# Kernel tuning notes

Hardware: AMD Instinct MI355X
Metric: run time of the kernel (lower is better)

The kernel has to match this reference:

```python
import jax, jax.numpy as jnp
import numpy as np

IGNORE = 255


def interp_bilinear_ac(x, H, W):
    """Bilinear interpolation with align_corners=True. x: [B,C,h,w] -> [B,C,H,W]."""
    B, C, h, w = x.shape

    def coords(n_in, n_out):
        s = jnp.linspace(0.0, n_in - 1.0, n_out)
        i0 = jnp.clip(jnp.floor(s).astype(jnp.int32), 0, n_in - 2)
        t = (s - i0).astype(x.dtype)
        return i0, t

    y0, ty = coords(h, H)
    x = x[:, :, y0, :] * (1.0 - ty)[None, None, :, None] + x[:, :, y0 + 1, :] * ty[None, None, :, None]
    x0, tx = coords(w, W)
    x = x[:, :, :, x0] * (1.0 - tx) + x[:, :, :, x0 + 1] * tx
    return x


def cross_entropy(logits, labels):
    """Mean CE over valid pixels. logits: [B,C,H,W], labels: [B,H,W] int."""
    C = logits.shape[1]
    logp = jax.nn.log_softmax(logits, axis=1)
    lab = jnp.clip(labels, 0, C - 1)
    nll = -jnp.take_along_axis(logp, lab[:, None], axis=1)[:, 0]  # [B,H,W]
    valid = (labels != IGNORE).astype(logits.dtype)
    return jnp.sum(nll * valid) / jnp.maximum(jnp.sum(valid), 1.0)


def lovasz_softmax_flat(probs_flat, labels_flat, valid):
    """Multi-class Lovasz-Softmax, only_present=True. probs_flat: [P,C], labels_flat: [P]."""
    P, C = probs_flat.shape
    classes = jnp.arange(C)
    fg = ((labels_flat[None, :] == classes[:, None]) & valid[None, :]).astype(probs_flat.dtype)  # [C,P]
    vf = jnp.broadcast_to(valid, (C, P)).astype(probs_flat.dtype)
    # invalid pixels get error -1 so descending sort puts them last
    errors = jnp.where(valid[None, :], jnp.abs(fg - probs_flat.T), -1.0)
    order = jnp.argsort(-errors, axis=1)
    err_s = jnp.take_along_axis(errors, order, axis=1)
    fg_s = jnp.take_along_axis(fg, order, axis=1)
    val_s = jnp.take_along_axis(vf, order, axis=1)
    gts = jnp.sum(fg_s, axis=1, keepdims=True)
    inter = gts - jnp.cumsum(fg_s, axis=1)
    union = gts + jnp.cumsum(val_s - fg_s, axis=1)
    jac = 1.0 - inter / jnp.maximum(union, 1.0)
    jac = jnp.concatenate([jac[:, :1], jac[:, 1:] - jac[:, :-1]], axis=1)
    per_class = jnp.sum(jnp.where(val_s > 0, err_s, 0.0) * jax.lax.stop_gradient(jac), axis=1)
    present = gts[:, 0] > 0
    n = jnp.maximum(jnp.sum(present.astype(probs_flat.dtype)), 1.0)
    return jnp.sum(jnp.where(present, per_class, 0.0)) / n


def lovasz_branch(logits, labels, H, W):
    p = jax.nn.softmax(interp_bilinear_ac(logits, H, W), axis=1)
    C = p.shape[1]
    probs_flat = jnp.transpose(p, (0, 2, 3, 1)).reshape(-1, C)
    labels_flat = labels.reshape(-1)
    return lovasz_softmax_flat(probs_flat, labels_flat, labels_flat != IGNORE)


def setup_inputs() -> dict:
    key = jax.random.key(0)
    ks = jax.random.split(key, 7)
    B, hs, ws, H, W = 4, 96, 96, 384, 384
    return {
        "preds0": jax.random.normal(ks[0], (B, 7, hs, ws), dtype=jnp.float32),
        "preds1": jax.random.normal(ks[1], (B, 3, hs, ws), dtype=jnp.float32),
        "preds2": jax.random.normal(ks[2], (B, 2, hs, ws), dtype=jnp.float32),
        "preds_dsn": jax.random.normal(ks[3], (B, 7, hs, ws), dtype=jnp.float32),
        "targets0": jax.random.randint(ks[4], (B, H, W), 0, 7, dtype=jnp.int32),
        "targets1": jax.random.randint(ks[5], (B, H, W), 0, 3, dtype=jnp.int32),
        "targets2": jax.random.randint(ks[6], (B, H, W), 0, 2, dtype=jnp.int32),
    }


def reference(preds0, preds1, preds2, preds_dsn, targets0, targets1, targets2):
    H, W = targets0.shape[1], targets0.shape[2]
    pred = interp_bilinear_ac(preds0, H, W)
    loss_ce = cross_entropy(pred, targets0)
    probs = jax.nn.softmax(pred, axis=1)
    C = probs.shape[1]
    probs_flat = jnp.transpose(probs, (0, 2, 3, 1)).reshape(-1, C)
    labels_flat = targets0.reshape(-1)
    loss = lovasz_softmax_flat(probs_flat, labels_flat, labels_flat != IGNORE)
    loss_hb = lovasz_branch(preds1, targets1, H, W)
    loss_fb = lovasz_branch(preds2, targets2, H, W)
    pred_dsn = interp_bilinear_ac(preds_dsn, H, W)
    loss_dsn = cross_entropy(pred_dsn, targets0)
    return loss_ce + loss + 0.4 * loss_hb + 0.4 * loss_fb + 0.4 * loss_dsn
```

## Files before the change

kernel.cpp:

```cpp
#include <hip/hip_runtime.h>

#define NBUCK 32
#define NCLS 12
#define NCHUNK 16
#define NBMAIN 1152
#define SPC (NBMAIN / NCHUNK)
#define NENT (NCLS * NBUCK)
#define IGNORE_LBL 255
#define PIX (4*384*384)

typedef float float4a __attribute__((ext_vector_type(4), aligned(4)));


__global__ __launch_bounds__(128) void k_main(
    const float* __restrict__ p0, const float* __restrict__ p1,
    const float* __restrict__ p2, const float* __restrict__ pdsn,
    const int* __restrict__ t0, const int* __restrict__ t1, const int* __restrict__ t2,
    unsigned int* __restrict__ slices, float4* __restrict__ ce_part)
{
    __shared__ unsigned int h[NENT];
    __shared__ float cw[2][3];
    int t = threadIdx.x;
    #pragma unroll
    for (int i = t; i < NENT; i += 128) h[i] = 0u;
    __syncthreads();

    int g = blockIdx.x * 128 + t;
    int gx = g % 96;
    int row = g / 96;
    int y = row % 384;
    int b = row / 384;
    int x4 = gx * 4;

    const float scale = 95.0f / 383.0f;
    float sy = y * scale;
    int y0 = (int)sy; if (y0 > 94) y0 = 94;
    float ty = sy - (float)y0;
    float oty = 1.0f - ty;
    float sx0 = (float)x4 * scale;
    int X0 = (int)sx0; if (X0 > 92) X0 = 92;

    float Wa[4][4], Wb[4][4];
    #pragma unroll
    for (int i = 0; i < 4; i++) {
        float sx = (float)(x4 + i) * scale;
        #pragma unroll
        for (int j = 0; j < 4; j++) {
            float w = fmaxf(1.0f - fabsf(sx - (float)(X0 + j)), 0.0f);
            Wa[i][j] = w * oty;
            Wb[i][j] = w * ty;
        }
    }

    const int rb = y0 * 96 + X0;

    auto interp4 = [&](const float* A, int c, float zout[4]) {
        float4a r0 = *(const float4a*)(A + c * 9216);
        float4a r1 = *(const float4a*)(A + c * 9216 + 96);
        #pragma unroll
        for (int i = 0; i < 4; i++) {
            zout[i] = r0.x*Wa[i][0] + r0.y*Wa[i][1] + r0.z*Wa[i][2] + r0.w*Wa[i][3]
                    + r1.x*Wb[i][0] + r1.y*Wb[i][1] + r1.z*Wb[i][2] + r1.w*Wb[i][3];
        }
    };
    auto histadd = [&](int cls, int fg, float err) {
        int bk = (int)(err * (float)NBUCK);
        if (bk > NBUCK - 1) bk = NBUCK - 1;
        atomicAdd(&h[cls * NBUCK + bk], 0x10000u | (unsigned)fg);
    };

    float nll = 0.f, nll2 = 0.f; int vc = 0;

    int4 L0 = *(const int4*)(t0 + g * 4);
    int l0v[4] = {L0.x, L0.y, L0.z, L0.w};

    {
        const float* A0 = p0 + b * 7 * 9216 + rb;
        float z0[7][4];
        #pragma unroll
        for (int c = 0; c < 7; c++) interp4(A0, c, z0[c]);
        #pragma unroll
        for (int i = 0; i < 4; i++) {
            int l = l0v[i];
            if (l != IGNORE_LBL) {
                float e[7]; e[0] = 1.0f; float s = 1.0f;
                #pragma unroll
                for (int c = 1; c < 7; c++) { e[c] = __expf(z0[c][i] - z0[0][i]); s += e[c]; }
                float inv = 1.0f / s;
                float zl = z0[0][i];
                #pragma unroll
                for (int c = 1; c < 7; c++) zl = (l == c) ? z0[c][i] : zl;
                nll += __logf(s) - (zl - z0[0][i]);
                vc++;
                #pragma unroll
                for (int c = 0; c < 7; c++) {
                    int fg = (l == c);
                    histadd(c, fg, fabsf((float)fg - e[c] * inv));
                }
            }
        }
    }

    {
        const float* Ad = pdsn + b * 7 * 9216 + rb;
        float zd[7][4];
        #pragma unroll
        for (int c = 0; c < 7; c++) interp4(Ad, c, zd[c]);
        #pragma unroll
        for (int i = 0; i < 4; i++) {
            int l = l0v[i];
            if (l != IGNORE_LBL) {
                float s = 1.0f;
                #pragma unroll
                for (int c = 1; c < 7; c++) s += __expf(zd[c][i] - zd[0][i]);
                float zl = zd[0][i];
                #pragma unroll
                for (int c = 1; c < 7; c++) zl = (l == c) ? zd[c][i] : zl;
                nll2 += __logf(s) - (zl - zd[0][i]);
            }
        }
    }

    {
        int4 L1 = *(const int4*)(t1 + g * 4);
        int l1v[4] = {L1.x, L1.y, L1.z, L1.w};
        const float* A1 = p1 + b * 3 * 9216 + rb;
        float z1[3][4];
        #pragma unroll
        for (int c = 0; c < 3; c++) interp4(A1, c, z1[c]);
        #pragma unroll
        for (int i = 0; i < 4; i++) {
            int l = l1v[i];
            if (l != IGNORE_LBL) {
                float e1 = __expf(z1[1][i] - z1[0][i]);
                float e2 = __expf(z1[2][i] - z1[0][i]);
                float inv = 1.0f / (1.0f + e1 + e2);
                histadd(7 + 0, (l == 0), fabsf((float)(l == 0) - inv));
                histadd(7 + 1, (l == 1), fabsf((float)(l == 1) - e1 * inv));
                histadd(7 + 2, (l == 2), fabsf((float)(l == 2) - e2 * inv));
            }
        }
    }

    {
        int4 L2 = *(const int4*)(t2 + g * 4);
        int l2v[4] = {L2.x, L2.y, L2.z, L2.w};
        const float* A2 = p2 + b * 2 * 9216 + rb;
        float z2a[2][4];
        #pragma unroll
        for (int c = 0; c < 2; c++) interp4(A2, c, z2a[c]);
        #pragma unroll
        for (int i = 0; i < 4; i++) {
            int l = l2v[i];
            if (l != IGNORE_LBL) {
                float p0c = 1.0f / (1.0f + __expf(z2a[1][i] - z2a[0][i]));
                histadd(10, (l == 0), fabsf((float)(l == 0) - p0c));
            }
        }
    }

    #pragma unroll
    for (int o = 32; o > 0; o >>= 1) {
        nll  += __shfl_down(nll, o);
        nll2 += __shfl_down(nll2, o);
        vc   += __shfl_down(vc, o);
    }
    int wv = t >> 6, ln = t & 63;
    if (ln == 0) { cw[wv][0] = nll; cw[wv][1] = nll2; cw[wv][2] = (float)vc; }
    __syncthreads();
    if (t == 0) {
        ce_part[blockIdx.x] = make_float4(cw[0][0] + cw[1][0],
                                          cw[0][1] + cw[1][1],
                                          cw[0][2] + cw[1][2], 0.f);
    }

    unsigned int* dst = slices + (size_t)blockIdx.x * NENT;
    #pragma unroll
    for (int i = t; i < NENT; i += 128) dst[i] = h[i];
}

__global__ __launch_bounds__(32) void k_merge(
    const unsigned int* __restrict__ slices, unsigned int* __restrict__ partial)
{
    int kk = blockIdx.x % NCLS;
    int cy = blockIdx.x / NCLS;
    int bk = threadIdx.x;
    int s0 = cy * SPC;
    unsigned int acc = 0;
    for (int s = 0; s < SPC; s++)
        acc += slices[(size_t)(s0 + s) * NENT + kk * NBUCK + bk];
    partial[(size_t)(cy * NCLS + kk) * NBUCK + bk] = acc;
}

__global__ __launch_bounds__(512) void k_fin(
    const unsigned int* __restrict__ partial, const float4* __restrict__ ce_part,
    float* __restrict__ out)
{
    int t = threadIdx.x;
    __shared__ float ce_tot[3];
    __shared__ float cwf[8][3];
    __shared__ unsigned long long sc[512];
    __shared__ float sf[512];
    __shared__ float cls_lov[NCLS];
    __shared__ float cls_pres[NCLS];

    float a = 0.f, bb = 0.f, cc = 0.f;
    for (int e = t; e < NBMAIN; e += 512) {
        float4 v = ce_part[e];
        a += v.x; bb += v.y; cc += v.z;
    }
    #pragma unroll
    for (int o = 32; o > 0; o >>= 1) {
        a += __shfl_down(a, o); bb += __shfl_down(bb, o); cc += __shfl_down(cc, o);
    }
    if ((t & 63) == 0) { cwf[t >> 6][0] = a; cwf[t >> 6][1] = bb; cwf[t >> 6][2] = cc; }
    __syncthreads();
    if (t == 0) {
        float x = 0.f, y = 0.f, z = 0.f;
        for (int w = 0; w < 8; w++) { x += cwf[w][0]; y += cwf[w][1]; z += cwf[w][2]; }
        ce_tot[0] = x; ce_tot[1] = y; ce_tot[2] = z;
    }

    int sub = t >> 5;
    int p   = t & 31;
    int bk  = NBUCK - 1 - p;

    int kk = sub;
    unsigned int cnt = 0, fg = 0;
    if (kk < NCLS) {
        int src = (kk == 11) ? 10 : kk;
        #pragma unroll
        for (int cy = 0; cy < NCHUNK; cy++) {
            unsigned int v = partial[(size_t)(cy * NCLS + src) * NBUCK + bk];
            cnt += v >> 16; fg += v & 0xffffu;
        }
        if (kk == 11) fg = cnt - fg;
    }
    unsigned long long own = ((unsigned long long)cnt << 32) | fg;
    sc[t] = own;
    __syncthreads();
    #pragma unroll
    for (int o = 1; o < 32; o <<= 1) {
        unsigned long long add = (p >= o) ? sc[t - o] : 0ull;
        __syncthreads();
        sc[t] += add;
        __syncthreads();
    }
    unsigned long long total = sc[(sub << 5) + 31];
    unsigned long long excl = sc[t] - own;
    unsigned int G = (unsigned int)(total & 0xffffffffu);

    float contrib = 0.f;
    if (G > 0 && cnt > 0) {
        unsigned int rr = (unsigned int)(excl >> 32);
        unsigned int F  = (unsigned int)(excl & 0xffffffffu);
        float fG = (float)G;
        float j0 = 1.0f - (fG - (float)F) / fmaxf(fG + (float)rr - (float)F, 1.0f);
        rr += cnt; F += fg;
        float j1 = 1.0f - (fG - (float)F) / fmaxf(fG + (float)rr - (float)F, 1.0f);
        contrib = (((float)bk + 0.5f) * (1.0f / (float)NBUCK)) * (j1 - j0);
    }
    sf[t] = contrib;
    __syncthreads();
    #pragma unroll
    for (int o = 16; o > 0; o >>= 1) {
        if (p < o) sf[t] += sf[t + o];
        __syncthreads();
    }
    if (p == 0 && kk < NCLS) {
        cls_lov[kk]  = (G > 0) ? sf[t] : 0.f;
        cls_pres[kk] = (G > 0) ? 1.f : 0.f;
    }
    __syncthreads();

    if (t == 0) {
        float l0 = 0.f, p0c = 0.f, l1 = 0.f, p1c = 0.f, l2 = 0.f, p2c = 0.f;
        for (int k = 0; k < 7;  k++) { l0 += cls_lov[k]; p0c += cls_pres[k]; }
        for (int k = 7; k < 10; k++) { l1 += cls_lov[k]; p1c += cls_pres[k]; }
        for (int k = 10; k < 12; k++) { l2 += cls_lov[k]; p2c += cls_pres[k]; }
        float vcnt = fmaxf(ce_tot[2], 1.0f);
        out[0] = ce_tot[0] / vcnt
               + l0 / fmaxf(p0c, 1.f)
               + 0.4f * (l1 / fmaxf(p1c, 1.f))
               + 0.4f * (l2 / fmaxf(p2c, 1.f))
               + 0.4f * (ce_tot[1] / vcnt);
    }
}

extern "C" void kernel_launch(void* const* d_in, const int* in_sizes, int n_in,
                              void* d_out, int out_size, void* d_ws, size_t ws_size,
                              hipStream_t stream)
{
    const float* p0 = (const float*)d_in[0];
    const float* p1 = (const float*)d_in[1];
    const float* p2 = (const float*)d_in[2];
    const float* pd = (const float*)d_in[3];
    const int* t0 = (const int*)d_in[4];
    const int* t1 = (const int*)d_in[5];
    const int* t2 = (const int*)d_in[6];

    char* ws = (char*)d_ws;
    const size_t partial_bytes = (size_t)NCHUNK * NENT * 4;
    const size_t cepart_bytes = (size_t)NBMAIN * 16;
    unsigned int* partial = (unsigned int*)ws;
    float4* ce_part = (float4*)(ws + partial_bytes);
    unsigned int* slices = (unsigned int*)(ws + partial_bytes + cepart_bytes);

    k_main<<<NBMAIN, 128, 0, stream>>>(p0, p1, p2, pd, t0, t1, t2, slices, ce_part);
    k_merge<<<NCLS * NCHUNK, 32, 0, stream>>>(slices, partial);
    k_fin<<<1, 512, 0, stream>>>(partial, ce_part, (float*)d_out);
}
```

Before: 25.59 us.

## Replace per-block histogram slices and merge kernel with atomic partial accumulation

Each main block now adds its shared-memory histogram into one of 16 partial buffers in global memory using atomics, replacing the per-block slice store and the separate merge kernel. A memset zeroes the partial buffers before the launch. The bilinear interpolation is also refactored to do the vertical blend first, then a 4-tap horizontal blend, which cuts the FMA count and register use. The cost is atomic contention on global memory plus one extra memset node, and packed counts per partial could overflow 16 bits if too many pixels land in one bucket.

```diff
diff --git a/kernel.cpp b/kernel.cpp
--- a/kernel.cpp
+++ b/kernel.cpp
@@ -2,9 +2,8 @@
 
 #define NBUCK 32
 #define NCLS 12
-#define NCHUNK 16
 #define NBMAIN 1152
-#define SPC (NBMAIN / NCHUNK)
+#define NPART 16
 #define NENT (NCLS * NBUCK)
 #define IGNORE_LBL 255
 #define PIX (4*384*384)
@@ -16,7 +15,7 @@
     const float* __restrict__ p0, const float* __restrict__ p1,
     const float* __restrict__ p2, const float* __restrict__ pdsn,
     const int* __restrict__ t0, const int* __restrict__ t1, const int* __restrict__ t2,
-    unsigned int* __restrict__ slices, float4* __restrict__ ce_part)
+    unsigned int* __restrict__ pcnt, float4* __restrict__ ce_part)
 {
     __shared__ unsigned int h[NENT];
     __shared__ float cw[2][3];
@@ -40,16 +39,13 @@
     float sx0 = (float)x4 * scale;
     int X0 = (int)sx0; if (X0 > 92) X0 = 92;
 
-    float Wa[4][4], Wb[4][4];
+    float W[4][4];
     #pragma unroll
     for (int i = 0; i < 4; i++) {
         float sx = (float)(x4 + i) * scale;
         #pragma unroll
-        for (int j = 0; j < 4; j++) {
-            float w = fmaxf(1.0f - fabsf(sx - (float)(X0 + j)), 0.0f);
-            Wa[i][j] = w * oty;
-            Wb[i][j] = w * ty;
-        }
+        for (int j = 0; j < 4; j++)
+            W[i][j] = fmaxf(1.0f - fabsf(sx - (float)(X0 + j)), 0.0f);
     }
 
     const int rb = y0 * 96 + X0;
@@ -57,11 +53,13 @@
     auto interp4 = [&](const float* A, int c, float zout[4]) {
         float4a r0 = *(const float4a*)(A + c * 9216);
         float4a r1 = *(const float4a*)(A + c * 9216 + 96);
-        #pragma unroll
-        for (int i = 0; i < 4; i++) {
-            zout[i] = r0.x*Wa[i][0] + r0.y*Wa[i][1] + r0.z*Wa[i][2] + r0.w*Wa[i][3]
-                    + r1.x*Wb[i][0] + r1.y*Wb[i][1] + r1.z*Wb[i][2] + r1.w*Wb[i][3];
-        }
+        float v0 = r0.x * oty + r1.x * ty;
+        float v1 = r0.y * oty + r1.y * ty;
+        float v2 = r0.z * oty + r1.z * ty;
+        float v3 = r0.w * oty + r1.w * ty;
+        #pragma unroll
+        for (int i = 0; i < 4; i++)
+            zout[i] = v0*W[i][0] + v1*W[i][1] + v2*W[i][2] + v3*W[i][3];
     };
     auto histadd = [&](int cls, int fg, float err) {
         int bk = (int)(err * (float)NBUCK);
@@ -174,26 +172,16 @@
                                           cw[0][2] + cw[1][2], 0.f);
     }
 
-    unsigned int* dst = slices + (size_t)blockIdx.x * NENT;
-    #pragma unroll
-    for (int i = t; i < NENT; i += 128) dst[i] = h[i];
+    unsigned int* pp = pcnt + (size_t)(blockIdx.x & (NPART - 1)) * NENT;
+    #pragma unroll
+    for (int i = t; i < NENT; i += 128) {
+        unsigned int v = h[i];
+        if (v) atomicAdd(&pp[i], v);
+    }
 }
 
-__global__ __launch_bounds__(32) void k_merge(
-    const unsigned int* __restrict__ slices, unsigned int* __restrict__ partial)
-{
-    int kk = blockIdx.x % NCLS;
-    int cy = blockIdx.x / NCLS;
-    int bk = threadIdx.x;
-    int s0 = cy * SPC;
-    unsigned int acc = 0;
-    for (int s = 0; s < SPC; s++)
-        acc += slices[(size_t)(s0 + s) * NENT + kk * NBUCK + bk];
-    partial[(size_t)(cy * NCLS + kk) * NBUCK + bk] = acc;
-}
-
 __global__ __launch_bounds__(512) void k_fin(
-    const unsigned int* __restrict__ partial, const float4* __restrict__ ce_part,
+    const unsigned int* __restrict__ pcnt, const float4* __restrict__ ce_part,
     float* __restrict__ out)
 {
     int t = threadIdx.x;
@@ -230,8 +218,8 @@
     if (kk < NCLS) {
         int src = (kk == 11) ? 10 : kk;
         #pragma unroll
-        for (int cy = 0; cy < NCHUNK; cy++) {
-            unsigned int v = partial[(size_t)(cy * NCLS + src) * NBUCK + bk];
+        for (int cy = 0; cy < NPART; cy++) {
+            unsigned int v = pcnt[(size_t)cy * NENT + src * NBUCK + bk];
             cnt += v >> 16; fg += v & 0xffffu;
         }
         if (kk == 11) fg = cnt - fg;
@@ -300,13 +288,12 @@
     const int* t2 = (const int*)d_in[6];
 
     char* ws = (char*)d_ws;
-    const size_t partial_bytes = (size_t)NCHUNK * NENT * 4;
-    const size_t cepart_bytes = (size_t)NBMAIN * 16;
-    unsigned int* partial = (unsigned int*)ws;
-    float4* ce_part = (float4*)(ws + partial_bytes);
-    unsigned int* slices = (unsigned int*)(ws + partial_bytes + cepart_bytes);
-
-    k_main<<<NBMAIN, 128, 0, stream>>>(p0, p1, p2, pd, t0, t1, t2, slices, ce_part);
-    k_merge<<<NCLS * NCHUNK, 32, 0, stream>>>(slices, partial);
-    k_fin<<<1, 512, 0, stream>>>(partial, ce_part, (float*)d_out);
+    const size_t pcnt_bytes = (size_t)NPART * NENT * 4;
+    unsigned int* pcnt = (unsigned int*)ws;
+    float4* ce_part = (float4*)(ws + pcnt_bytes);
+
+    hipMemsetAsync(d_ws, 0, pcnt_bytes, stream);
+
+    k_main<<<NBMAIN, 128, 0, stream>>>(p0, p1, p2, pd, t0, t1, t2, pcnt, ce_part);
+    k_fin<<<1, 512, 0, stream>>>(pcnt, ce_part, (float*)d_out);
 }
```

Result: faster. 24.98 us (median of 2 runs) (-2.4%).
